# Kernel optimization log

Hardware: AMD Instinct MI355X
Metric: run time of the kernel (lower is better)

Reference implementation:

```python
import jax, jax.numpy as jnp
import numpy as np

N_NODES = 50000
N_EDGES = 800000
IN_CH, HID_CH, OUT_CH = 128, 256, 128
BN_EPS = 1e-5


def gcn_conv(x, W, b, src, dst):
    """PyG GCNConv: h = x @ W; symmetric normalization with self-loops; scatter-add; + bias."""
    N = x.shape[0]
    h = x @ W  # [N, out_ch]
    # degree including self-loop (all edge weights = 1)
    deg = jax.ops.segment_sum(jnp.ones(src.shape[0], h.dtype), dst, num_segments=N) + 1.0
    dis = jax.lax.rsqrt(deg)  # deg^-1/2
    norm = dis[src] * dis[dst]  # [E]
    agg = jax.ops.segment_sum(h[src] * norm[:, None], dst, num_segments=N)
    # self-loop contribution: norm_ii = dis[i]^2
    return agg + h * (dis * dis)[:, None] + b


def batchnorm_train(x, gamma, beta):
    mu = jnp.mean(x, axis=0)
    var = jnp.mean((x - mu) ** 2, axis=0)  # biased var, as torch BN uses for normalization
    return (x - mu) * jax.lax.rsqrt(var + BN_EPS) * gamma + beta


def setup_inputs() -> dict:
    key = jax.random.key(0)
    ks = jax.random.split(key, 4)
    x = jax.random.normal(ks[0], (N_NODES, IN_CH), dtype=jnp.float32)
    edge_index = jax.random.randint(ks[1], (2, N_EDGES), 0, N_NODES, dtype=jnp.int64 if jax.config.jax_enable_x64 else jnp.int32)
    W1 = jax.random.normal(ks[2], (IN_CH, HID_CH), dtype=jnp.float32) * (1.0 / np.sqrt(IN_CH))
    W2 = jax.random.normal(ks[3], (HID_CH, OUT_CH), dtype=jnp.float32) * (1.0 / np.sqrt(HID_CH))
    return {
        "x": x,
        "edge_index": edge_index,
        "W1": W1,
        "b1": jnp.zeros((HID_CH,), jnp.float32),
        "gamma1": jnp.ones((HID_CH,), jnp.float32),
        "beta1": jnp.zeros((HID_CH,), jnp.float32),
        "W2": W2,
        "b2": jnp.zeros((OUT_CH,), jnp.float32),
    }


def reference(x, edge_index, W1, b1, gamma1, beta1, W2, b2):
    src, dst = edge_index[0], edge_index[1]
    h = gcn_conv(x, W1, b1, src, dst)
    h = jax.nn.relu(batchnorm_train(h, gamma1, beta1))
    # dropout omitted (deterministic eval-style reference)
    return gcn_conv(h, W2, b2, src, dst)
```

## Files before the change

kernel.cpp:

```cpp
#include <hip/hip_runtime.h>

#define N_NODES 50000
#define N_EDGES 800000
#define C_IN 128
#define C_HID 256
#define C_OUT 128
#define BN_EPS 1e-5f

typedef __bf16 v8bf __attribute__((ext_vector_type(8)));
typedef float f32x4 __attribute__((ext_vector_type(4)));

static __device__ __forceinline__ unsigned short f2bf(float f) {
    unsigned int u = __float_as_uint(f);
    u += 0x7fffu + ((u >> 16) & 1u);
    return (unsigned short)(u >> 16);
}
static __device__ __forceinline__ float bf2f(unsigned short h) {
    return __uint_as_float((unsigned int)h << 16);
}
static __device__ __forceinline__ unsigned int pack2(float a, float b) {
    return (unsigned int)f2bf(a) | ((unsigned int)f2bf(b) << 16);
}
static __device__ __forceinline__ float lo2f(unsigned int u) { return __uint_as_float(u << 16); }
static __device__ __forceinline__ float hi2f(unsigned int u) { return __uint_as_float(u & 0xffff0000u); }

#define DEG_BLOCKS ((N_EDGES + 255) / 256)


__global__ __launch_bounds__(256) void k_deg_wtrans(const int* __restrict__ dst, int* __restrict__ deg,
                                                    const float* __restrict__ W1, const float* __restrict__ W2,
                                                    unsigned short* __restrict__ WT1, unsigned short* __restrict__ WT2) {
    int bx = blockIdx.x, t = threadIdx.x;
    if (bx < DEG_BLOCKS) {
        int e = bx * 256 + t;
        if (e < N_EDGES) atomicAdd(&deg[dst[e]], 1);
    } else {
        int i = (bx - DEG_BLOCKS) * 256 + t;
        if (i < C_IN * C_HID) {
            int n = i >> 7, k = i & 127;
            WT1[n * C_IN + k] = f2bf(W1[k * C_HID + n]);
        } else {
            int j = i - C_IN * C_HID;
            int n = j >> 8, k = j & 255;
            WT2[n * C_HID + k] = f2bf(W2[k * C_OUT + n]);
        }
    }
}


__global__ __launch_bounds__(512) void k_scan1(const int* __restrict__ deg, int* __restrict__ rs,
                                               int* __restrict__ partial, float* __restrict__ dis) {
    __shared__ int s[512];
    int t = threadIdx.x;
    int i = blockIdx.x * 512 + t;
    int v = (i < N_NODES) ? deg[i] : 0;
    if (i < N_NODES) dis[i] = rsqrtf((float)v + 1.0f);
    s[t] = v;
    __syncthreads();
    for (int off = 1; off < 512; off <<= 1) {
        int tv = (t >= off) ? s[t - off] : 0;
        __syncthreads();
        s[t] += tv;
        __syncthreads();
    }
    if (i < N_NODES) rs[i + 1] = s[t];
    if (t == 511) partial[blockIdx.x] = s[511];
}

__global__ __launch_bounds__(256) void k_scan23(int* __restrict__ rs, const int* __restrict__ partial,
                                                int* __restrict__ cur, int nb) {
    __shared__ int pre[128];
    __shared__ int wsum[2];
    int t = threadIdx.x;
    int lane = t & 63;
    int pv = 0, v = 0;
    if (t < 128) {
        pv = (t < nb) ? partial[t] : 0;
        v = pv;
#pragma unroll
        for (int off = 1; off < 64; off <<= 1) {
            int u = __shfl_up(v, off);
            if (lane >= off) v += u;
        }
        if (lane == 63) wsum[t >> 6] = v;
    }
    __syncthreads();
    if (t < 128) {
        if (t >= 64) v += wsum[0];
        pre[t] = v - pv;
    }
    __syncthreads();
    int i = blockIdx.x * 256 + t;
    if (i < N_NODES) {
        int vv = rs[i + 1] + pre[i >> 9];
        rs[i + 1] = vv;
        cur[i + 1] = vv;
    }
    if (i == 0) { rs[0] = 0; cur[0] = 0; }
}


#define SCAT_GROUPS 256
#define NODES_PER_SLICE (N_NODES / 8)
#define EDGES_PER_CHUNK ((N_EDGES + SCAT_GROUPS - 1) / SCAT_GROUPS)
#define SCAT_BLOCKS (SCAT_GROUPS * 8)

__global__ __launch_bounds__(256) void k_scatter_xscale(const int* __restrict__ src, const int* __restrict__ dst,
                                                        int* __restrict__ cur, int* __restrict__ eidx,
                                                        const float* __restrict__ x, const float* __restrict__ dis,
                                                        unsigned short* __restrict__ xs) {
    int bx = blockIdx.x, t = threadIdx.x;
    if (bx < SCAT_BLOCKS) {
        int slice = bx & 7;
        int g = bx >> 3;
        int lo = slice * NODES_PER_SLICE;
        int hi = lo + NODES_PER_SLICE;
        int e0 = g * EDGES_PER_CHUNK;
        int e1 = e0 + EDGES_PER_CHUNK;
        if (e1 > N_EDGES) e1 = N_EDGES;
        for (int e = e0 + t; e < e1; e += 256) {
            int d = dst[e];
            if (d >= lo && d < hi) {
                int pos = atomicAdd(&cur[d], 1);
                eidx[pos] = src[e];
            }
        }
    } else {
        int i = (bx - SCAT_BLOCKS) * 256 + t;
        int node = i >> 4;
        if (node < N_NODES) {
            int g8 = (i & 15) * 8;
            float d = dis[node];
            float4 v0 = *(const float4*)&x[(size_t)node * C_IN + g8];
            float4 v1 = *(const float4*)&x[(size_t)node * C_IN + g8 + 4];
            uint4 o = make_uint4(pack2(v0.x * d, v0.y * d), pack2(v0.z * d, v0.w * d),
                                 pack2(v1.x * d, v1.y * d), pack2(v1.z * d, v1.w * d));
            *(uint4*)&xs[(size_t)node * C_IN + g8] = o;
        }
    }
}


template <bool FINAL>
__global__ __launch_bounds__(256) void k_aggr(const unsigned short* __restrict__ g,
                                              const float* __restrict__ dis, const float* __restrict__ bias,
                                              const int* __restrict__ rs, const int* __restrict__ eidx,
                                              unsigned short* __restrict__ outb, float* __restrict__ outf) {
    int wid = (blockIdx.x * 256 + threadIdx.x) >> 6;
    int lane = threadIdx.x & 63;
    if (wid >= N_NODES) return;
    int slot = lane >> 5;
    int cp = lane & 31;
    int s = rs[wid], e = rs[wid + 1];
    float a0 = 0.f, a1 = 0.f, a2 = 0.f, a3 = 0.f;
    float c0 = 0.f, c1 = 0.f, c2 = 0.f, c3 = 0.f;
    int p = s;
    for (; p + 7 < e; p += 8) {
        int i0 = eidx[p + slot];
        int i1 = eidx[p + 2 + slot];
        int i2 = eidx[p + 4 + slot];
        int i3 = eidx[p + 6 + slot];
        ushort4 v0 = *(const ushort4*)&g[(size_t)i0 * 128 + cp * 4];
        ushort4 v1 = *(const ushort4*)&g[(size_t)i1 * 128 + cp * 4];
        ushort4 v2 = *(const ushort4*)&g[(size_t)i2 * 128 + cp * 4];
        ushort4 v3 = *(const ushort4*)&g[(size_t)i3 * 128 + cp * 4];
        a0 += bf2f(v0.x) + bf2f(v1.x); a1 += bf2f(v0.y) + bf2f(v1.y);
        a2 += bf2f(v0.z) + bf2f(v1.z); a3 += bf2f(v0.w) + bf2f(v1.w);
        c0 += bf2f(v2.x) + bf2f(v3.x); c1 += bf2f(v2.y) + bf2f(v3.y);
        c2 += bf2f(v2.z) + bf2f(v3.z); c3 += bf2f(v2.w) + bf2f(v3.w);
    }
    for (; p + 1 < e; p += 2) {
        int i0 = eidx[p + slot];
        ushort4 v0 = *(const ushort4*)&g[(size_t)i0 * 128 + cp * 4];
        a0 += bf2f(v0.x); a1 += bf2f(v0.y); a2 += bf2f(v0.z); a3 += bf2f(v0.w);
    }
    if (p < e && slot == 0) {
        int i0 = eidx[p];
        ushort4 v0 = *(const ushort4*)&g[(size_t)i0 * 128 + cp * 4];
        a0 += bf2f(v0.x); a1 += bf2f(v0.y); a2 += bf2f(v0.z); a3 += bf2f(v0.w);
    }
    a0 += c0; a1 += c1; a2 += c2; a3 += c3;
    a0 += __shfl_xor(a0, 32); a1 += __shfl_xor(a1, 32);
    a2 += __shfl_xor(a2, 32); a3 += __shfl_xor(a3, 32);
    if (slot == 0) {
        ushort4 gi = *(const ushort4*)&g[(size_t)wid * 128 + cp * 4];
        float d = dis[wid];
        if (FINAL) {
            float4 bv = *(const float4*)&bias[cp * 4];
            float4 o = make_float4(fmaf(d, a0 + bf2f(gi.x), bv.x), fmaf(d, a1 + bf2f(gi.y), bv.y),
                                   fmaf(d, a2 + bf2f(gi.z), bv.z), fmaf(d, a3 + bf2f(gi.w), bv.w));
            *(float4*)&outf[(size_t)wid * 128 + cp * 4] = o;
        } else {
            ushort4 z;
            z.x = f2bf(d * (a0 + bf2f(gi.x)));
            z.y = f2bf(d * (a1 + bf2f(gi.y)));
            z.z = f2bf(d * (a2 + bf2f(gi.z)));
            z.w = f2bf(d * (a3 + bf2f(gi.w)));
            *(ushort4*)&outb[(size_t)wid * 128 + cp * 4] = z;
        }
    }
}


template <bool TRANS, int KC>
__global__ __launch_bounds__(256, 2) void k_gemmv(const unsigned short* __restrict__ Ah,
                                                  const unsigned short* __restrict__ BT,
                                                  unsigned short* __restrict__ C,
                                                  const float* __restrict__ dis, const float* __restrict__ bias,
                                                  float* __restrict__ bnsum, float* __restrict__ bnsq,
                                                  const float* __restrict__ gamma, const float* __restrict__ beta,
                                                  int M, int N) {
    constexpr int K = KC * 32;
    constexpr int BP = K + 8;
    __shared__ unsigned short Blds[64 * BP];
    __shared__ float tsc_s[K];
    __shared__ float tof_s[K];

    int t = threadIdx.x;
    int w = t >> 6, lane = t & 63;
    int lm = lane & 15, quad = lane >> 4;
    int col0 = blockIdx.y * 64;

    if (TRANS && t < K) {
        float inv_n = 1.0f / (float)N_NODES;
        float mu = bnsum[t] * inv_n;
        float var = bnsq[t] * inv_n - mu * mu;
        float a = gamma[t] * rsqrtf(var + BN_EPS);
        tsc_s[t] = a;
        tof_s[t] = beta[t] - mu * a;
    }
    constexpr int NLD = 64 * K / 8;
    for (int j = t; j < NLD; j += 256) {
        int n = j / (K / 8);
        int kq = j % (K / 8);
        *(uint4*)&Blds[n * BP + kq * 8] = *(const uint4*)&BT[(size_t)(col0 + n) * K + kq * 8];
    }
    __syncthreads();
    v8bf bfr[4][KC];
#pragma unroll
    for (int in = 0; in < 4; ++in)
#pragma unroll
        for (int kc = 0; kc < KC; ++kc)
            bfr[in][kc] = *(const v8bf*)&Blds[(in * 16 + lm) * BP + kc * 32 + quad * 8];
    __syncthreads();

    unsigned short* Ct = Blds + w * (16 * 80);

    float bias_r[4];
    if (!TRANS) {
#pragma unroll
        for (int in = 0; in < 4; ++in) bias_r[in] = bias[col0 + in * 16 + lm];
    }
    float ss[4] = {0.f, 0.f, 0.f, 0.f}, qq[4] = {0.f, 0.f, 0.f, 0.f};

    int strip0 = (blockIdx.x * 4 + w) * 4;
#pragma unroll
    for (int s = 0; s < 4; ++s) {
        int strip = strip0 + s;
        if (strip * 16 >= M) break;
        int arow = strip * 16 + lm;
        uint4 araw[KC];
#pragma unroll
        for (int kc = 0; kc < KC; ++kc)
            araw[kc] = *(const uint4*)&Ah[(size_t)arow * K + kc * 32 + quad * 8];
        float dqa[4];
        if (TRANS) *(float4*)dqa = *(const float4*)&dis[strip * 16 + quad * 4];
        f32x4 acc[4] = {};
#pragma unroll
        for (int kc = 0; kc < KC; ++kc) {
            v8bf af;
            if (TRANS) {
                int kb2 = kc * 32 + quad * 8;
                float4 s0 = *(const float4*)&tsc_s[kb2];
                float4 s1 = *(const float4*)&tsc_s[kb2 + 4];
                float4 o0 = *(const float4*)&tof_s[kb2];
                float4 o1 = *(const float4*)&tof_s[kb2 + 4];
                uint4 h = araw[kc];
                float f0 = fmaxf(fmaf(lo2f(h.x), s0.x, o0.x), 0.f);
                float f1 = fmaxf(fmaf(hi2f(h.x), s0.y, o0.y), 0.f);
                float f2 = fmaxf(fmaf(lo2f(h.y), s0.z, o0.z), 0.f);
                float f3 = fmaxf(fmaf(hi2f(h.y), s0.w, o0.w), 0.f);
                float f4 = fmaxf(fmaf(lo2f(h.z), s1.x, o1.x), 0.f);
                float f5 = fmaxf(fmaf(hi2f(h.z), s1.y, o1.y), 0.f);
                float f6 = fmaxf(fmaf(lo2f(h.w), s1.z, o1.z), 0.f);
                float f7 = fmaxf(fmaf(hi2f(h.w), s1.w, o1.w), 0.f);
                uint4 pk = make_uint4(pack2(f0, f1), pack2(f2, f3), pack2(f4, f5), pack2(f6, f7));
                af = *(v8bf*)&pk;
            } else {
                af = *(v8bf*)&araw[kc];
            }
#pragma unroll
            for (int in = 0; in < 4; ++in)
                acc[in] = __builtin_amdgcn_mfma_f32_16x16x32_bf16(af, bfr[in][kc], acc[in], 0, 0, 0);
        }
#pragma unroll
        for (int in = 0; in < 4; ++in) {
#pragma unroll
            for (int q = 0; q < 4; ++q) {
                float val = TRANS ? acc[in][q] * dqa[q] : acc[in][q] + bias_r[in];
                unsigned short hb = f2bf(val);
                Ct[(quad * 4 + q) * 80 + in * 16 + lm] = hb;
                if (!TRANS) {
                    float v = bf2f(hb);
                    ss[in] += v;
                    qq[in] = fmaf(v, v, qq[in]);
                }
            }
        }
#pragma unroll
        for (int it = 0; it < 2; ++it) {
            int rl = (lane >> 3) + it * 8;
            uint4 v = *(const uint4*)&Ct[rl * 80 + (lane & 7) * 8];
            *(uint4*)&C[(size_t)(strip * 16 + rl) * N + col0 + (lane & 7) * 8] = v;
        }
    }
    if (!TRANS) {
#pragma unroll
        for (int in = 0; in < 4; ++in) {
            float s = ss[in], q2 = qq[in];
            s += __shfl_xor(s, 16); q2 += __shfl_xor(q2, 16);
            s += __shfl_xor(s, 32); q2 += __shfl_xor(q2, 32);
            if (quad == 0) {
                atomicAdd(&bnsum[col0 + in * 16 + lm], s);
                atomicAdd(&bnsq[col0 + in * 16 + lm], q2);
            }
        }
    }
}


extern "C" void kernel_launch(void* const* d_in, const int* in_sizes, int n_in,
                              void* d_out, int out_size, void* d_ws, size_t ws_size,
                              hipStream_t stream) {
    const float* x      = (const float*)d_in[0];
    const int*   ei     = (const int*)d_in[1];
    const float* W1     = (const float*)d_in[2];
    const float* b1     = (const float*)d_in[3];
    const float* gamma1 = (const float*)d_in[4];
    const float* beta1  = (const float*)d_in[5];
    const float* W2     = (const float*)d_in[6];
    const float* b2     = (const float*)d_in[7];
    const int* srcv = ei;
    const int* dstv = ei + N_EDGES;
    float* out = (float*)d_out;

    char* w = (char*)d_ws;
    size_t off = 0;
    auto alloc = [&](size_t bytes) {
        void* p = w + off;
        off = (off + bytes + 255) & ~(size_t)255;
        return p;
    };
    int*   deg     = (int*)alloc(N_NODES * 4);
    float* bnsum   = (float*)alloc(256 * 4);
    float* bnsq    = (float*)alloc(256 * 4);
    size_t zero_bytes = off;
    float* dis     = (float*)alloc(N_NODES * 4);
    int*   rs      = (int*)alloc((N_NODES + 1) * 4);
    int*   cur     = (int*)alloc((N_NODES + 1) * 4);
    int*   partial = (int*)alloc(128 * 4);
    int*   eidx    = (int*)alloc((size_t)N_EDGES * 4);
    unsigned short* WT1 = (unsigned short*)alloc((size_t)C_IN * C_HID * 2);
    unsigned short* WT2 = (unsigned short*)alloc((size_t)C_HID * C_OUT * 2);
    unsigned short* xs  = (unsigned short*)alloc((size_t)N_NODES * C_IN * 2);
    unsigned short* P   = (unsigned short*)alloc((size_t)N_NODES * C_IN * 2);
    unsigned short* z1  = (unsigned short*)alloc((size_t)N_NODES * C_HID * 2);
    unsigned short* g2  = (unsigned short*)alloc((size_t)N_NODES * C_OUT * 2);
    (void)ws_size; (void)in_sizes; (void)n_in; (void)out_size;

    hipMemsetAsync(deg, 0, zero_bytes, stream);

    int nb = (N_NODES + 511) / 512;
    k_deg_wtrans<<<DEG_BLOCKS + 256, 256, 0, stream>>>(dstv, deg, W1, W2, WT1, WT2);
    k_scan1<<<nb, 512, 0, stream>>>(deg, rs, partial, dis);
    k_scan23<<<(N_NODES + 255) / 256, 256, 0, stream>>>(rs, partial, cur, nb);
    k_scatter_xscale<<<SCAT_BLOCKS + (N_NODES * 16 + 255) / 256, 256, 0, stream>>>(
        srcv, dstv, cur, eidx, x, dis, xs);

    k_aggr<false><<<(N_NODES * 64 + 255) / 256, 256, 0, stream>>>(xs, dis, nullptr, rs, eidx, P, nullptr);
    dim3 gg1((N_NODES + 255) / 256, C_HID / 64);
    k_gemmv<false, 4><<<gg1, 256, 0, stream>>>(P, WT1, z1, nullptr, b1, bnsum, bnsq, nullptr, nullptr,
                                               N_NODES, C_HID);

    dim3 gg2((N_NODES + 255) / 256, C_OUT / 64);
    k_gemmv<true, 8><<<gg2, 256, 0, stream>>>(z1, WT2, g2, dis, nullptr, bnsum, bnsq, gamma1, beta1,
                                              N_NODES, C_OUT);
    k_aggr<true><<<(N_NODES * 64 + 255) / 256, 256, 0, stream>>>(g2, dis, b2, rs, eidx, nullptr, out);
}
```

Measured before the change: 286.4 us.

## Build CSR via atomic ranks from degree pass instead of second atomic scatter

The degree-count kernel now stores each edge's atomicAdd return value as its rank within its destination bucket. The CSR fill becomes an atomic-free placement at rs[dst]+rank using vectorized int4 loads, replacing the sliced scatter that re-read all edges eight times and did a second round of atomics. It adds a 3.2 MB rank buffer write and read. The slot order within each row now depends on atomic ordering, which can change float summation order.

```diff
diff --git a/kernel.cpp b/kernel.cpp
--- a/kernel.cpp
+++ b/kernel.cpp
@@ -28,12 +28,13 @@
 
 
 __global__ __launch_bounds__(256) void k_deg_wtrans(const int* __restrict__ dst, int* __restrict__ deg,
+                                                    int* __restrict__ rank,
                                                     const float* __restrict__ W1, const float* __restrict__ W2,
                                                     unsigned short* __restrict__ WT1, unsigned short* __restrict__ WT2) {
     int bx = blockIdx.x, t = threadIdx.x;
     if (bx < DEG_BLOCKS) {
         int e = bx * 256 + t;
-        if (e < N_EDGES) atomicAdd(&deg[dst[e]], 1);
+        if (e < N_EDGES) rank[e] = atomicAdd(&deg[dst[e]], 1);
     } else {
         int i = (bx - DEG_BLOCKS) * 256 + t;
         if (i < C_IN * C_HID) {
@@ -68,7 +69,7 @@
 }
 
 __global__ __launch_bounds__(256) void k_scan23(int* __restrict__ rs, const int* __restrict__ partial,
-                                                int* __restrict__ cur, int nb) {
+                                                int nb) {
     __shared__ int pre[128];
     __shared__ int wsum[2];
     int t = threadIdx.x;
@@ -92,41 +93,34 @@
     __syncthreads();
     int i = blockIdx.x * 256 + t;
     if (i < N_NODES) {
-        int vv = rs[i + 1] + pre[i >> 9];
-        rs[i + 1] = vv;
-        cur[i + 1] = vv;
-    }
-    if (i == 0) { rs[0] = 0; cur[0] = 0; }
-}
-
-
-#define SCAT_GROUPS 256
-#define NODES_PER_SLICE (N_NODES / 8)
-#define EDGES_PER_CHUNK ((N_EDGES + SCAT_GROUPS - 1) / SCAT_GROUPS)
-#define SCAT_BLOCKS (SCAT_GROUPS * 8)
-
-__global__ __launch_bounds__(256) void k_scatter_xscale(const int* __restrict__ src, const int* __restrict__ dst,
-                                                        int* __restrict__ cur, int* __restrict__ eidx,
-                                                        const float* __restrict__ x, const float* __restrict__ dis,
-                                                        unsigned short* __restrict__ xs) {
+        rs[i + 1] = rs[i + 1] + pre[i >> 9];
+    }
+    if (i == 0) rs[0] = 0;
+}
+
+
+#define PLACE_BLOCKS ((N_EDGES / 4 + 255) / 256)
+
+__global__ __launch_bounds__(256) void k_place_xscale(const int* __restrict__ src, const int* __restrict__ dst,
+                                                      const int* __restrict__ rank, const int* __restrict__ rs,
+                                                      int* __restrict__ eidx,
+                                                      const float* __restrict__ x, const float* __restrict__ dis,
+                                                      unsigned short* __restrict__ xs) {
     int bx = blockIdx.x, t = threadIdx.x;
-    if (bx < SCAT_BLOCKS) {
-        int slice = bx & 7;
-        int g = bx >> 3;
-        int lo = slice * NODES_PER_SLICE;
-        int hi = lo + NODES_PER_SLICE;
-        int e0 = g * EDGES_PER_CHUNK;
-        int e1 = e0 + EDGES_PER_CHUNK;
-        if (e1 > N_EDGES) e1 = N_EDGES;
-        for (int e = e0 + t; e < e1; e += 256) {
-            int d = dst[e];
-            if (d >= lo && d < hi) {
-                int pos = atomicAdd(&cur[d], 1);
-                eidx[pos] = src[e];
-            }
+    if (bx < PLACE_BLOCKS) {
+        int q = bx * 256 + t;
+        int e = q * 4;
+        if (e < N_EDGES) {
+            int4 d4 = *(const int4*)&dst[e];
+            int4 r4 = *(const int4*)&rank[e];
+            int4 s4 = *(const int4*)&src[e];
+            eidx[rs[d4.x] + r4.x] = s4.x;
+            eidx[rs[d4.y] + r4.y] = s4.y;
+            eidx[rs[d4.z] + r4.z] = s4.z;
+            eidx[rs[d4.w] + r4.w] = s4.w;
         }
     } else {
-        int i = (bx - SCAT_BLOCKS) * 256 + t;
+        int i = (bx - PLACE_BLOCKS) * 256 + t;
         int node = i >> 4;
         if (node < N_NODES) {
             int g8 = (i & 15) * 8;
@@ -357,7 +351,7 @@
     size_t zero_bytes = off;
     float* dis     = (float*)alloc(N_NODES * 4);
     int*   rs      = (int*)alloc((N_NODES + 1) * 4);
-    int*   cur     = (int*)alloc((N_NODES + 1) * 4);
+    int*   rank    = (int*)alloc((size_t)N_EDGES * 4);
     int*   partial = (int*)alloc(128 * 4);
     int*   eidx    = (int*)alloc((size_t)N_EDGES * 4);
     unsigned short* WT1 = (unsigned short*)alloc((size_t)C_IN * C_HID * 2);
@@ -368,14 +362,14 @@
     unsigned short* g2  = (unsigned short*)alloc((size_t)N_NODES * C_OUT * 2);
     (void)ws_size; (void)in_sizes; (void)n_in; (void)out_size;
 
-    hipMemsetAsync(deg, 0, zero_bytes, stream);
+    (void)hipMemsetAsync(deg, 0, zero_bytes, stream);
 
     int nb = (N_NODES + 511) / 512;
-    k_deg_wtrans<<<DEG_BLOCKS + 256, 256, 0, stream>>>(dstv, deg, W1, W2, WT1, WT2);
+    k_deg_wtrans<<<DEG_BLOCKS + 256, 256, 0, stream>>>(dstv, deg, rank, W1, W2, WT1, WT2);
     k_scan1<<<nb, 512, 0, stream>>>(deg, rs, partial, dis);
-    k_scan23<<<(N_NODES + 255) / 256, 256, 0, stream>>>(rs, partial, cur, nb);
-    k_scatter_xscale<<<SCAT_BLOCKS + (N_NODES * 16 + 255) / 256, 256, 0, stream>>>(
-        srcv, dstv, cur, eidx, x, dis, xs);
+    k_scan23<<<(N_NODES + 255) / 256, 256, 0, stream>>>(rs, partial, nb);
+    k_place_xscale<<<PLACE_BLOCKS + (N_NODES * 16 + 255) / 256, 256, 0, stream>>>(
+        srcv, dstv, rank, rs, eidx, x, dis, xs);
 
     k_aggr<false><<<(N_NODES * 64 + 255) / 256, 256, 0, stream>>>(xs, dis, nullptr, rs, eidx, P, nullptr);
     dim3 gg1((N_NODES + 255) / 256, C_HID / 64);
```

Measured after the change: 264.7 us. 7.6% less time.
